# Optimization experiments

Measured on AMD Instinct MI355X. Metric: run time of the kernel, lower is better.

## Reference

```python
import jax, jax.numpy as jnp
import numpy as np

N = 50000      # occupied sparse voxels
C_IN = 512     # inplanes (= 4*planes for residual)
P = 128        # planes
K = 27         # 3x3x3 kernel volume in 3D
EPS = 1e-5
NEG = 0.1      # leaky-relu slope


def setup_inputs() -> dict:
    key = jax.random.key(0)
    k1, k2, k3, k4, k5, k6 = jax.random.split(key, 6)
    x = jax.random.normal(k1, (N, C_IN), dtype=jnp.float32)
    mask = (jax.random.uniform(k2, (N, 1)) > 0.3).astype(jnp.float32)
    nbr = jax.random.randint(k3, (N, K), 0, N, dtype=jnp.int32)
    W1 = jax.random.normal(k4, (C_IN, P), dtype=jnp.float32) * (1.0 / np.sqrt(C_IN))
    W2 = jax.random.normal(k5, (K, P, P), dtype=jnp.float32) * (1.0 / np.sqrt(K * P))
    W3 = jax.random.normal(k6, (P, C_IN), dtype=jnp.float32) * (1.0 / np.sqrt(P))
    return {"x": x, "mask": mask, "nbr": nbr, "W1": W1, "W2": W2, "W3": W3}


def lrelu(x):
    return jnp.where(x >= 0, x, NEG * x)


def inorm(x):
    # Minkowski instance norm: per-channel over all points of the instance
    mu = jnp.mean(x, axis=0, keepdims=True)
    var = jnp.var(x, axis=0, keepdims=True)
    return (x - mu) * jax.lax.rsqrt(var + EPS)


def pconv_k1(x, m, W):
    # 1x1x1 partial conv: mask, matmul, renormalize by coverage (=m itself)
    valid = (m > 0).astype(x.dtype)          # [N,1]
    return (x @ W) * valid, valid


def pconv_k3(x, m, nbr, W):
    # gather-GEMM partial conv over 27-neighborhood map
    mg = m[nbr]                                # [N,K,1]
    xg = x[nbr] * mg                           # [N,K,P] masked gather
    out = jnp.einsum('nkc,kcd->nd', xg, W)     # [N,P]
    msum = jnp.sum(mg, axis=1)                 # [N,1] coverage count
    ratio = (K / jnp.maximum(msum, 1.0)) * (msum > 0).astype(x.dtype)
    return out * ratio, (msum > 0).astype(x.dtype)


def reference(x, mask, nbr, W1, W2, W3):
    out, m = pconv_k1(x, mask, W1)
    out = lrelu(inorm(out))
    out, m = pconv_k3(out, m, nbr, W2)
    out = lrelu(inorm(out))
    out, m = pconv_k1(out, m, W3)
    out = inorm(out)
    out = lrelu(out + x)                       # residual (no downsample)
    m = jnp.clip(m + mask, 0.0, 1.0)           # mask residual + clamp
    return out, m
```

## Files before the change

kernel.cpp:

```cpp
#include <hip/hip_runtime.h>
#include <hip/hip_bf16.h>

#define NPTS 50000
#define CIN  512
#define PCH  128
#define KNB  27
#define EPSV 1e-5f
#define NEGS 0.1f

typedef __bf16 bf16;
typedef __bf16 bf16x8 __attribute__((ext_vector_type(8)));
typedef __bf16 bf16x4 __attribute__((ext_vector_type(4)));
typedef float  f32x4  __attribute__((ext_vector_type(4)));

typedef void __attribute__((address_space(3)))* as3ptr;
typedef const void __attribute__((address_space(1)))* as1ptr;
__device__ __forceinline__ void gl_lds16(const void* g, void* l) {
  __builtin_amdgcn_global_load_lds((as1ptr)g, (as3ptr)l, 16, 0, 0);
}


__global__ void xcvt_kernel(const float* __restrict__ x, bf16* __restrict__ xb) {
  int i = (blockIdx.x * blockDim.x + threadIdx.x) * 8;
  if (i >= NPTS * CIN) return;
  float4 a = *(const float4*)&x[i];
  float4 b = *(const float4*)&x[i + 4];
  bf16x8 o;
  o[0] = (bf16)a.x; o[1] = (bf16)a.y; o[2] = (bf16)a.z; o[3] = (bf16)a.w;
  o[4] = (bf16)b.x; o[5] = (bf16)b.y; o[6] = (bf16)b.z; o[7] = (bf16)b.w;
  *(bf16x8*)&xb[i] = o;
}

__global__ void tcvt_kernel(const float* __restrict__ src, bf16* __restrict__ dst,
                            int R, int Ccols) {
  int i = blockIdx.x * blockDim.x + threadIdx.x;
  if (i >= R * Ccols) return;
  int c = i / R, r = i - c * R;
  dst[i] = (bf16)src[(size_t)r * Ccols + c];
}

__global__ void tcvt_w2k_kernel(const float* __restrict__ src, bf16* __restrict__ dst) {
  int i = blockIdx.x * blockDim.x + threadIdx.x;
  if (i >= KNB * PCH * PCH) return;
  int k = i >> 14, rem = i & 16383;
  int d = rem >> 7, c = rem & 127;
  dst[i] = (bf16)src[(k << 14) + c * 128 + d];
}

__global__ void prep_kernel(const int* __restrict__ nbr, const float* __restrict__ mask,
                            int* __restrict__ nbrT, float* __restrict__ ratio,
                            float* __restrict__ valid2) {
  int n = blockIdx.x * blockDim.x + threadIdx.x;
  if (n >= NPTS) return;
  float s = 0.f;
#pragma unroll
  for (int k = 0; k < KNB; ++k) {
    int idx = nbr[n * KNB + k];
    nbrT[k * NPTS + n] = idx;
    s += (mask[idx] > 0.f) ? 1.f : 0.f;
  }
  ratio[n]  = s > 0.f ? 27.0f / s : 0.f;
  valid2[n] = s > 0.f ? 1.f : 0.f;
}

__global__ void finalize_kernel(const float* __restrict__ ssum, const float* __restrict__ ssq,
                                float* __restrict__ mu, float* __restrict__ inv) {
  int c = threadIdx.x;
  float m = ssum[c] / (float)NPTS;
  float v = ssq[c] / (float)NPTS - m * m;
  mu[c]  = m;
  inv[c] = rsqrtf(v + EPSV);
}

__global__ void ew_kernel(const float* __restrict__ in, const float* __restrict__ mu,
                          const float* __restrict__ inv, const float* __restrict__ rowmask,
                          bf16* __restrict__ outb) {
  int i = (blockIdx.x * blockDim.x + threadIdx.x) * 4;
  if (i >= NPTS * PCH) return;
  float4 v = *(const float4*)&in[i];
  int c = i & 127;
  int row = i >> 7;
  float mk = rowmask[row];
  float t0 = (v.x - mu[c + 0]) * inv[c + 0];
  float t1 = (v.y - mu[c + 1]) * inv[c + 1];
  float t2 = (v.z - mu[c + 2]) * inv[c + 2];
  float t3 = (v.w - mu[c + 3]) * inv[c + 3];
  t0 = (t0 >= 0.f ? t0 : NEGS * t0) * mk;
  t1 = (t1 >= 0.f ? t1 : NEGS * t1) * mk;
  t2 = (t2 >= 0.f ? t2 : NEGS * t2) * mk;
  t3 = (t3 >= 0.f ? t3 : NEGS * t3) * mk;
  bf16x4 o;
  o[0] = (bf16)t0; o[1] = (bf16)t1; o[2] = (bf16)t2; o[3] = (bf16)t3;
  *(bf16x4*)&outb[i] = o;
}

__global__ void final_kernel(const float* __restrict__ x, const bf16* __restrict__ out3n,
                             const float* __restrict__ mu, const float* __restrict__ inv,
                             float* __restrict__ out) {
  int i = (blockIdx.x * blockDim.x + threadIdx.x) * 8;
  if (i >= NPTS * CIN) return;
  bf16x8 v = *(const bf16x8*)&out3n[i];
  float4 x0 = *(const float4*)&x[i];
  float4 x1 = *(const float4*)&x[i + 4];
  int c = i & 511;
  float t[8];
  float xv[8] = {x0.x, x0.y, x0.z, x0.w, x1.x, x1.y, x1.z, x1.w};
#pragma unroll
  for (int q = 0; q < 8; ++q) {
    float u = ((float)v[q] - mu[c + q]) * inv[c + q] + xv[q];
    t[q] = u >= 0.f ? u : NEGS * u;
  }
  float4 o0 = {t[0], t[1], t[2], t[3]}, o1 = {t[4], t[5], t[6], t[7]};
  *(float4*)&out[i] = o0;
  *(float4*)&out[i + 4] = o1;
}

__global__ void maskout_kernel(const float* __restrict__ mask, const float* __restrict__ valid2,
                               float* __restrict__ outm) {
  int n = blockIdx.x * blockDim.x + threadIdx.x;
  if (n >= NPTS) return;
  outm[n] = fminf(valid2[n] + mask[n], 1.f);
}


__global__ __launch_bounds__(256) void gemm1_kernel(
    const bf16* __restrict__ xb, const bf16* __restrict__ w1t,
    const float* __restrict__ mask, float* __restrict__ out1,
    float* __restrict__ ssum, float* __restrict__ ssq) {
  __shared__ __align__(16) bf16 As[2][128 * 128];
  int row0 = blockIdx.x * 128;
  int tid = threadIdx.x;
  int lane = tid & 63, wid = tid >> 6;
  int mq = (wid >> 1) * 64, nq = (wid & 1) * 64;
  int lr = lane & 15, lq = lane >> 4;
  int rb = tid >> 4;
  int msw = (tid & 15) ^ (rb & 7);
  int rowc[8];
#pragma unroll
  for (int j = 0; j < 8; ++j) {
    int rr = row0 + rb + 16 * j;
    rowc[j] = rr < NPTS ? rr : NPTS - 1;
  }
  f32x4 acc[4][4];
#pragma unroll
  for (int i = 0; i < 4; ++i)
#pragma unroll
    for (int j = 0; j < 4; ++j)
#pragma unroll
      for (int r = 0; r < 4; ++r) acc[i][j][r] = 0.f;

#pragma unroll
  for (int j = 0; j < 8; ++j)
    gl_lds16(xb + (size_t)rowc[j] * CIN + (msw << 3),
             &As[0][(j * 256 + wid * 64) * 8]);
  __syncthreads();

  for (int kc = 0; kc < 4; ++kc) {
    int cur = kc & 1;
    const bf16* bp = w1t + (size_t)(nq + lr) * CIN + kc * 128 + lq * 8;
    bf16x8 bfg[4][4];
#pragma unroll
    for (int c0i = 0; c0i < 4; ++c0i)
#pragma unroll
      for (int i = 0; i < 4; ++i)
        bfg[c0i][i] = *(const bf16x8*)(bp + (size_t)i * 16 * CIN + c0i * 32);
    if (kc < 3) {
#pragma unroll
      for (int j = 0; j < 8; ++j)
        gl_lds16(xb + (size_t)rowc[j] * CIN + (kc + 1) * 128 + (msw << 3),
                 &As[cur ^ 1][(j * 256 + wid * 64) * 8]);
    }
#pragma unroll
    for (int c0i = 0; c0i < 4; ++c0i) {
      int cs = ((c0i << 2) + lq) ^ (lr & 7);
      bf16x8 af[4];
#pragma unroll
      for (int i = 0; i < 4; ++i) af[i] = *(const bf16x8*)&As[cur][(mq + i * 16 + lr) * 128 + cs * 8];
#pragma unroll
      for (int i = 0; i < 4; ++i)
#pragma unroll
        for (int j = 0; j < 4; ++j)
          acc[i][j] = __builtin_amdgcn_mfma_f32_16x16x32_bf16(af[i], bfg[c0i][j], acc[i][j], 0, 0, 0);
    }
    __syncthreads();
  }
  float rs[4][4];
#pragma unroll
  for (int i = 0; i < 4; ++i)
#pragma unroll
    for (int r = 0; r < 4; ++r) {
      int row = row0 + mq + i * 16 + lq * 4 + r;
      rs[i][r] = (row < NPTS) ? (mask[row] > 0.f ? 1.f : 0.f) : 0.f;
    }
#pragma unroll
  for (int j = 0; j < 4; ++j) {
    int col = nq + j * 16 + lr;
    float s = 0.f, q = 0.f;
#pragma unroll
    for (int i = 0; i < 4; ++i) {
#pragma unroll
      for (int r = 0; r < 4; ++r) {
        int row = row0 + mq + i * 16 + lq * 4 + r;
        if (row < NPTS) {
          float v = acc[i][j][r] * rs[i][r];
          out1[(size_t)row * PCH + col] = v;
          s += v; q += v * v;
        }
      }
    }
    s += __shfl_xor(s, 16); s += __shfl_xor(s, 32);
    q += __shfl_xor(q, 16); q += __shfl_xor(q, 32);
    if (lq == 0) { atomicAdd(&ssum[col], s); atomicAdd(&ssq[col], q); }
  }
}

__global__ __launch_bounds__(256) void gemm2_kernel(
    const bf16* __restrict__ a, const bf16* __restrict__ w2k,
    const int* __restrict__ nbrT, const float* __restrict__ ratio,
    float* __restrict__ out2, float* __restrict__ ssum, float* __restrict__ ssq) {
  __shared__ __align__(16) bf16 As[2][128 * 128];
  int row0 = blockIdx.x * 128;
  int tid = threadIdx.x;
  int lane = tid & 63, wid = tid >> 6;
  int mq = (wid >> 1) * 64, nq = (wid & 1) * 64;
  int lr = lane & 15, lq = lane >> 4;
  int rb = tid >> 4;
  int msw = (tid & 15) ^ (rb & 7);
  int rowc[8];
#pragma unroll
  for (int j = 0; j < 8; ++j) {
    int rr = row0 + rb + 16 * j;
    rowc[j] = rr < NPTS ? rr : NPTS - 1;
  }
  f32x4 acc[4][4];
#pragma unroll
  for (int i = 0; i < 4; ++i)
#pragma unroll
    for (int j = 0; j < 4; ++j)
#pragma unroll
      for (int r = 0; r < 4; ++r) acc[i][j][r] = 0.f;

  int nidx[8];
#pragma unroll
  for (int j = 0; j < 8; ++j) nidx[j] = nbrT[rowc[j]];
#pragma unroll
  for (int j = 0; j < 8; ++j)
    gl_lds16(a + (size_t)nidx[j] * PCH + (msw << 3),
             &As[0][(j * 256 + wid * 64) * 8]);
#pragma unroll
  for (int j = 0; j < 8; ++j) nidx[j] = nbrT[NPTS + rowc[j]];
  __syncthreads();

  for (int k = 0; k < KNB; ++k) {
    int cur = k & 1;
    const bf16* bp = w2k + (size_t)k * PCH * PCH + (nq + lr) * PCH + lq * 8;
    bf16x8 bfg[4][4];
#pragma unroll
    for (int c0i = 0; c0i < 4; ++c0i)
#pragma unroll
      for (int i = 0; i < 4; ++i)
        bfg[c0i][i] = *(const bf16x8*)(bp + (size_t)i * 16 * PCH + c0i * 32);
    if (k + 1 < KNB) {
#pragma unroll
      for (int j = 0; j < 8; ++j)
        gl_lds16(a + (size_t)nidx[j] * PCH + (msw << 3),
                 &As[cur ^ 1][(j * 256 + wid * 64) * 8]);
    }
    if (k + 2 < KNB) {
#pragma unroll
      for (int j = 0; j < 8; ++j) nidx[j] = nbrT[(k + 2) * NPTS + rowc[j]];
    }
#pragma unroll
    for (int c0i = 0; c0i < 4; ++c0i) {
      int cs = ((c0i << 2) + lq) ^ (lr & 7);
      bf16x8 af[4];
#pragma unroll
      for (int i = 0; i < 4; ++i) af[i] = *(const bf16x8*)&As[cur][(mq + i * 16 + lr) * 128 + cs * 8];
#pragma unroll
      for (int i = 0; i < 4; ++i)
#pragma unroll
        for (int j = 0; j < 4; ++j)
          acc[i][j] = __builtin_amdgcn_mfma_f32_16x16x32_bf16(af[i], bfg[c0i][j], acc[i][j], 0, 0, 0);
    }
    __syncthreads();
  }
  float rs[4][4];
#pragma unroll
  for (int i = 0; i < 4; ++i)
#pragma unroll
    for (int r = 0; r < 4; ++r) {
      int row = row0 + mq + i * 16 + lq * 4 + r;
      rs[i][r] = (row < NPTS) ? ratio[row] : 0.f;
    }
#pragma unroll
  for (int j = 0; j < 4; ++j) {
    int col = nq + j * 16 + lr;
    float s = 0.f, q = 0.f;
#pragma unroll
    for (int i = 0; i < 4; ++i) {
#pragma unroll
      for (int r = 0; r < 4; ++r) {
        int row = row0 + mq + i * 16 + lq * 4 + r;
        if (row < NPTS) {
          float v = acc[i][j][r] * rs[i][r];
          out2[(size_t)row * PCH + col] = v;
          s += v; q += v * v;
        }
      }
    }
    s += __shfl_xor(s, 16); s += __shfl_xor(s, 32);
    q += __shfl_xor(q, 16); q += __shfl_xor(q, 32);
    if (lq == 0) { atomicAdd(&ssum[col], s); atomicAdd(&ssq[col], q); }
  }
}

__global__ __launch_bounds__(256) void gemm3_kernel(
    const bf16* __restrict__ a, const bf16* __restrict__ w3t, bf16* __restrict__ out3n,
    float* __restrict__ ssum, float* __restrict__ ssq) {
  __shared__ __align__(16) bf16 As[128 * 128];
  int row0 = blockIdx.x * 128;
  int ncol0 = blockIdx.y * 128;
  int tid = threadIdx.x;
  int lane = tid & 63, wid = tid >> 6;
  int mq = (wid >> 1) * 64, nq = (wid & 1) * 64;
  int lr = lane & 15, lq = lane >> 4;
  int rb = tid >> 4;
  int msw = (tid & 15) ^ (rb & 7);
#pragma unroll
  for (int j = 0; j < 8; ++j) {
    int rr = row0 + rb + 16 * j;
    int rc = rr < NPTS ? rr : NPTS - 1;
    gl_lds16(a + (size_t)rc * PCH + (msw << 3),
             &As[(j * 256 + wid * 64) * 8]);
  }
  const bf16* bp = w3t + (size_t)(ncol0 + nq + lr) * PCH + lq * 8;
  bf16x8 bfg[4][4];
#pragma unroll
  for (int c0i = 0; c0i < 4; ++c0i)
#pragma unroll
    for (int i = 0; i < 4; ++i)
      bfg[c0i][i] = *(const bf16x8*)(bp + (size_t)i * 16 * PCH + c0i * 32);
  f32x4 acc[4][4];
#pragma unroll
  for (int i = 0; i < 4; ++i)
#pragma unroll
    for (int j = 0; j < 4; ++j)
#pragma unroll
      for (int r = 0; r < 4; ++r) acc[i][j][r] = 0.f;
  __syncthreads();
#pragma unroll
  for (int c0i = 0; c0i < 4; ++c0i) {
    int cs = ((c0i << 2) + lq) ^ (lr & 7);
    bf16x8 af[4];
#pragma unroll
    for (int i = 0; i < 4; ++i) af[i] = *(const bf16x8*)&As[(mq + i * 16 + lr) * 128 + cs * 8];
#pragma unroll
    for (int i = 0; i < 4; ++i)
#pragma unroll
      for (int j = 0; j < 4; ++j)
        acc[i][j] = __builtin_amdgcn_mfma_f32_16x16x32_bf16(af[i], bfg[c0i][j], acc[i][j], 0, 0, 0);
  }
#pragma unroll
  for (int j = 0; j < 4; ++j) {
    int col = ncol0 + nq + j * 16 + lr;
    float s = 0.f, q = 0.f;
#pragma unroll
    for (int i = 0; i < 4; ++i) {
#pragma unroll
      for (int r = 0; r < 4; ++r) {
        int row = row0 + mq + i * 16 + lq * 4 + r;
        if (row < NPTS) {
          float v = acc[i][j][r];
          out3n[(size_t)row * CIN + col] = (bf16)v;
          s += v; q += v * v;
        }
      }
    }
    s += __shfl_xor(s, 16); s += __shfl_xor(s, 32);
    q += __shfl_xor(q, 16); q += __shfl_xor(q, 32);
    if (lq == 0) { atomicAdd(&ssum[col], s); atomicAdd(&ssq[col], q); }
  }
}

extern "C" void kernel_launch(void* const* d_in, const int* in_sizes, int n_in,
                              void* d_out, int out_size, void* d_ws, size_t ws_size,
                              hipStream_t stream) {
  const float* x    = (const float*)d_in[0];
  const float* mask = (const float*)d_in[1];
  const int*   nbr  = (const int*)d_in[2];
  const float* W1   = (const float*)d_in[3];
  const float* W2   = (const float*)d_in[4];
  const float* W3   = (const float*)d_in[5];
  float* out = (float*)d_out;
  char* ws = (char*)d_ws;

  auto al = [](size_t x_) { return (x_ + 255) & ~(size_t)255; };
  size_t off = 0;
  size_t OFF_OUT1  = off; off += al((size_t)NPTS * PCH * 4);
  size_t OFF_OUT2  = off; off += al((size_t)NPTS * PCH * 4);
  size_t OFF_OUT1N = off; off += al((size_t)NPTS * PCH * 2);
  size_t OFF_OUT2N = off; off += al((size_t)NPTS * PCH * 2);
  size_t OFF_W1T   = off; off += al((size_t)PCH * CIN * 2);
  size_t OFF_W2K   = off; off += al((size_t)KNB * PCH * PCH * 2);
  size_t OFF_W3T   = off; off += al((size_t)CIN * PCH * 2);
  size_t OFF_NBRT  = off; off += al((size_t)KNB * NPTS * 4);
  size_t OFF_RATIO = off; off += al((size_t)NPTS * 4);
  size_t OFF_VAL2  = off; off += al((size_t)NPTS * 4);
  size_t OFF_SUMS  = off; off += al((size_t)1536 * 4);
  size_t OFF_PRMS  = off; off += al((size_t)1536 * 4);

  float* out1   = (float*)(ws + OFF_OUT1);
  float* out2   = (float*)(ws + OFF_OUT2);
  bf16*  out3n  = (bf16*)(ws + OFF_OUT1);
  bf16*  xb     = (bf16*)(ws + OFF_OUT2);
  bf16*  out1n  = (bf16*)(ws + OFF_OUT1N);
  bf16*  out2n  = (bf16*)(ws + OFF_OUT2N);
  bf16*  w1t    = (bf16*)(ws + OFF_W1T);
  bf16*  w2k    = (bf16*)(ws + OFF_W2K);
  bf16*  w3t    = (bf16*)(ws + OFF_W3T);
  int*   nbrT   = (int*)(ws + OFF_NBRT);
  float* ratio  = (float*)(ws + OFF_RATIO);
  float* valid2 = (float*)(ws + OFF_VAL2);
  float* sums   = (float*)(ws + OFF_SUMS);
  float* s1sum = sums, *s1sq = sums + 128;
  float* s2sum = sums + 256, *s2sq = sums + 384;
  float* s3sum = sums + 512, *s3sq = sums + 1024;
  float* prms = (float*)(ws + OFF_PRMS);
  float* mu1 = prms, *inv1 = prms + 128;
  float* mu2 = prms + 256, *inv2 = prms + 384;
  float* mu3 = prms + 512, *inv3 = prms + 1024;

  hipMemsetAsync(sums, 0, 1536 * 4, stream);

  prep_kernel<<<(NPTS + 255) / 256, 256, 0, stream>>>(nbr, mask, nbrT, ratio, valid2);
  tcvt_kernel<<<(CIN * PCH + 255) / 256, 256, 0, stream>>>(W1, w1t, CIN, PCH);
  tcvt_w2k_kernel<<<(KNB * PCH * PCH + 255) / 256, 256, 0, stream>>>(W2, w2k);
  tcvt_kernel<<<(PCH * CIN + 255) / 256, 256, 0, stream>>>(W3, w3t, PCH, CIN);
  xcvt_kernel<<<(NPTS * CIN / 8 + 255) / 256, 256, 0, stream>>>(x, xb);

  int mblocks = (NPTS + 127) / 128;

  gemm1_kernel<<<mblocks, 256, 0, stream>>>(xb, w1t, mask, out1, s1sum, s1sq);
  finalize_kernel<<<1, 128, 0, stream>>>(s1sum, s1sq, mu1, inv1);
  ew_kernel<<<(NPTS * PCH / 4 + 255) / 256, 256, 0, stream>>>(out1, mu1, inv1, mask, out1n);

  gemm2_kernel<<<mblocks, 256, 0, stream>>>(out1n, w2k, nbrT, ratio, out2, s2sum, s2sq);
  finalize_kernel<<<1, 128, 0, stream>>>(s2sum, s2sq, mu2, inv2);
  ew_kernel<<<(NPTS * PCH / 4 + 255) / 256, 256, 0, stream>>>(out2, mu2, inv2, valid2, out2n);

  dim3 g3(mblocks, 4);
  gemm3_kernel<<<g3, 256, 0, stream>>>(out2n, w3t, out3n, s3sum, s3sq);
  finalize_kernel<<<1, 512, 0, stream>>>(s3sum, s3sq, mu3, inv3);
  final_kernel<<<(NPTS * CIN / 8 + 255) / 256, 256, 0, stream>>>(x, out3n, mu3, inv3, out);
  maskout_kernel<<<(NPTS + 255) / 256, 256, 0, stream>>>(mask, valid2, out + (size_t)NPTS * CIN);
}
```

Baseline: 502.3 us.

## Restructure gemm1/gemm2 as single-wave 32-row tiles with shuffled gather indices

Gemm1 and gemm2 now run as one 64-thread wavefront per block over 32 rows and all 128 output columns, replacing four waves over a 128x128 tile. LDS use drops to a single 8 KB buffer with no __syncthreads, and the next gather is issued after the current A fragments are read into registers. In gemm2 the neighbour indices are loaded once per lane and spread with __shfl instead of 8 scalar loads per thread. The aim is more blocks, higher occupancy and fewer barriers, at the cost of reloading B weights from global per block, which raises weight traffic about fourfold, and less overlap because each iteration waits on vmcnt(0).

```diff
diff --git a/kernel.cpp b/kernel.cpp
--- a/kernel.cpp
+++ b/kernel.cpp
@@ -123,191 +123,197 @@
 }
 
 
-__global__ __launch_bounds__(256) void gemm1_kernel(
+__global__ __launch_bounds__(64, 3) void gemm1_kernel(
     const bf16* __restrict__ xb, const bf16* __restrict__ w1t,
     const float* __restrict__ mask, float* __restrict__ out1,
     float* __restrict__ ssum, float* __restrict__ ssq) {
-  __shared__ __align__(16) bf16 As[2][128 * 128];
-  int row0 = blockIdx.x * 128;
-  int tid = threadIdx.x;
-  int lane = tid & 63, wid = tid >> 6;
-  int mq = (wid >> 1) * 64, nq = (wid & 1) * 64;
+  __shared__ __align__(16) bf16 As[32 * 128];
+  int row0 = blockIdx.x * 32;
+  int lane = threadIdx.x;
   int lr = lane & 15, lq = lane >> 4;
-  int rb = tid >> 4;
-  int msw = (tid & 15) ^ (rb & 7);
-  int rowc[8];
+  int rowj[8];
 #pragma unroll
   for (int j = 0; j < 8; ++j) {
-    int rr = row0 + rb + 16 * j;
-    rowc[j] = rr < NPTS ? rr : NPTS - 1;
-  }
-  f32x4 acc[4][4];
-#pragma unroll
-  for (int i = 0; i < 4; ++i)
-#pragma unroll
-    for (int j = 0; j < 4; ++j)
-#pragma unroll
-      for (int r = 0; r < 4; ++r) acc[i][j][r] = 0.f;
-
-#pragma unroll
-  for (int j = 0; j < 8; ++j)
-    gl_lds16(xb + (size_t)rowc[j] * CIN + (msw << 3),
-             &As[0][(j * 256 + wid * 64) * 8]);
-  __syncthreads();
-
+    int rr = row0 + j * 4 + lq;
+    rowj[j] = rr < NPTS ? rr : NPTS - 1;
+  }
+  f32x4 acc[2][8];
+#pragma unroll
+  for (int i = 0; i < 2; ++i)
+#pragma unroll
+    for (int n = 0; n < 8; ++n)
+#pragma unroll
+      for (int r = 0; r < 4; ++r) acc[i][n][r] = 0.f;
+
+#pragma unroll
+  for (int j = 0; j < 8; ++j) {
+    int swz = lr ^ ((j & 1) * 4 + lq);
+    gl_lds16(xb + (size_t)rowj[j] * CIN + swz * 8, &As[j * 512 + lane * 8]);
+  }
+
+#pragma unroll 1
   for (int kc = 0; kc < 4; ++kc) {
-    int cur = kc & 1;
-    const bf16* bp = w1t + (size_t)(nq + lr) * CIN + kc * 128 + lq * 8;
-    bf16x8 bfg[4][4];
-#pragma unroll
-    for (int c0i = 0; c0i < 4; ++c0i)
-#pragma unroll
-      for (int i = 0; i < 4; ++i)
-        bfg[c0i][i] = *(const bf16x8*)(bp + (size_t)i * 16 * CIN + c0i * 32);
+    asm volatile("s_waitcnt vmcnt(0)" ::: "memory");
+    __builtin_amdgcn_sched_barrier(0);
+    bf16x8 af[2][4];
+#pragma unroll
+    for (int i = 0; i < 2; ++i)
+#pragma unroll
+      for (int c = 0; c < 4; ++c)
+        af[i][c] = *(const bf16x8*)&As[(i * 16 + lr) * 128 + (((c << 2) + lq) ^ (lr & 7)) * 8];
+    asm volatile("s_waitcnt lgkmcnt(0)" ::: "memory");
+    __builtin_amdgcn_sched_barrier(0);
+    const bf16* bp = w1t + (size_t)lr * CIN + kc * 128 + lq * 8;
+    bf16x8 bfg[8];
+#pragma unroll
+    for (int n = 0; n < 8; ++n) bfg[n] = *(const bf16x8*)(bp + (size_t)n * 16 * CIN);
+    __builtin_amdgcn_sched_barrier(0);
     if (kc < 3) {
 #pragma unroll
-      for (int j = 0; j < 8; ++j)
-        gl_lds16(xb + (size_t)rowc[j] * CIN + (kc + 1) * 128 + (msw << 3),
-                 &As[cur ^ 1][(j * 256 + wid * 64) * 8]);
-    }
-#pragma unroll
-    for (int c0i = 0; c0i < 4; ++c0i) {
-      int cs = ((c0i << 2) + lq) ^ (lr & 7);
-      bf16x8 af[4];
-#pragma unroll
-      for (int i = 0; i < 4; ++i) af[i] = *(const bf16x8*)&As[cur][(mq + i * 16 + lr) * 128 + cs * 8];
-#pragma unroll
-      for (int i = 0; i < 4; ++i)
-#pragma unroll
-        for (int j = 0; j < 4; ++j)
-          acc[i][j] = __builtin_amdgcn_mfma_f32_16x16x32_bf16(af[i], bfg[c0i][j], acc[i][j], 0, 0, 0);
-    }
-    __syncthreads();
-  }
-  float rs[4][4];
-#pragma unroll
-  for (int i = 0; i < 4; ++i)
+      for (int j = 0; j < 8; ++j) {
+        int swz = lr ^ ((j & 1) * 4 + lq);
+        gl_lds16(xb + (size_t)rowj[j] * CIN + (kc + 1) * 128 + swz * 8, &As[j * 512 + lane * 8]);
+      }
+    }
+    __builtin_amdgcn_sched_barrier(0);
+#pragma unroll
+    for (int n = 0; n < 8; ++n) {
+      acc[0][n] = __builtin_amdgcn_mfma_f32_16x16x32_bf16(af[0][0], bfg[n], acc[0][n], 0, 0, 0);
+      acc[1][n] = __builtin_amdgcn_mfma_f32_16x16x32_bf16(af[1][0], bfg[n], acc[1][n], 0, 0, 0);
+    }
+#pragma unroll
+    for (int c = 1; c < 4; ++c) {
+#pragma unroll
+      for (int n = 0; n < 8; ++n) bfg[n] = *(const bf16x8*)(bp + (size_t)n * 16 * CIN + c * 32);
+#pragma unroll
+      for (int n = 0; n < 8; ++n) {
+        acc[0][n] = __builtin_amdgcn_mfma_f32_16x16x32_bf16(af[0][c], bfg[n], acc[0][n], 0, 0, 0);
+        acc[1][n] = __builtin_amdgcn_mfma_f32_16x16x32_bf16(af[1][c], bfg[n], acc[1][n], 0, 0, 0);
+      }
+    }
+  }
+  float rs[2][4];
+#pragma unroll
+  for (int i = 0; i < 2; ++i)
 #pragma unroll
     for (int r = 0; r < 4; ++r) {
-      int row = row0 + mq + i * 16 + lq * 4 + r;
+      int row = row0 + i * 16 + lq * 4 + r;
       rs[i][r] = (row < NPTS) ? (mask[row] > 0.f ? 1.f : 0.f) : 0.f;
     }
 #pragma unroll
-  for (int j = 0; j < 4; ++j) {
-    int col = nq + j * 16 + lr;
+  for (int n = 0; n < 8; ++n) {
+    int col = n * 16 + lr;
     float s = 0.f, q = 0.f;
 #pragma unroll
-    for (int i = 0; i < 4; ++i) {
+    for (int i = 0; i < 2; ++i)
 #pragma unroll
       for (int r = 0; r < 4; ++r) {
-        int row = row0 + mq + i * 16 + lq * 4 + r;
+        int row = row0 + i * 16 + lq * 4 + r;
         if (row < NPTS) {
-          float v = acc[i][j][r] * rs[i][r];
+          float v = acc[i][n][r] * rs[i][r];
           out1[(size_t)row * PCH + col] = v;
           s += v; q += v * v;
         }
       }
-    }
     s += __shfl_xor(s, 16); s += __shfl_xor(s, 32);
     q += __shfl_xor(q, 16); q += __shfl_xor(q, 32);
     if (lq == 0) { atomicAdd(&ssum[col], s); atomicAdd(&ssq[col], q); }
   }
 }
 
-__global__ __launch_bounds__(256) void gemm2_kernel(
+__global__ __launch_bounds__(64, 3) void gemm2_kernel(
     const bf16* __restrict__ a, const bf16* __restrict__ w2k,
     const int* __restrict__ nbrT, const float* __restrict__ ratio,
     float* __restrict__ out2, float* __restrict__ ssum, float* __restrict__ ssq) {
-  __shared__ __align__(16) bf16 As[2][128 * 128];
-  int row0 = blockIdx.x * 128;
-  int tid = threadIdx.x;
-  int lane = tid & 63, wid = tid >> 6;
-  int mq = (wid >> 1) * 64, nq = (wid & 1) * 64;
+  __shared__ __align__(16) bf16 As[32 * 128];
+  int row0 = blockIdx.x * 32;
+  int lane = threadIdx.x;
   int lr = lane & 15, lq = lane >> 4;
-  int rb = tid >> 4;
-  int msw = (tid & 15) ^ (rb & 7);
-  int rowc[8];
+  int rglob = row0 + (lane & 31);
+  if (rglob >= NPTS) rglob = NPTS - 1;
+  f32x4 acc[2][8];
+#pragma unroll
+  for (int i = 0; i < 2; ++i)
+#pragma unroll
+    for (int n = 0; n < 8; ++n)
+#pragma unroll
+      for (int r = 0; r < 4; ++r) acc[i][n][r] = 0.f;
+
+  int idxreg = nbrT[rglob];
 #pragma unroll
   for (int j = 0; j < 8; ++j) {
-    int rr = row0 + rb + 16 * j;
-    rowc[j] = rr < NPTS ? rr : NPTS - 1;
-  }
-  f32x4 acc[4][4];
-#pragma unroll
-  for (int i = 0; i < 4; ++i)
-#pragma unroll
-    for (int j = 0; j < 4; ++j)
-#pragma unroll
-      for (int r = 0; r < 4; ++r) acc[i][j][r] = 0.f;
-
-  int nidx[8];
-#pragma unroll
-  for (int j = 0; j < 8; ++j) nidx[j] = nbrT[rowc[j]];
-#pragma unroll
-  for (int j = 0; j < 8; ++j)
-    gl_lds16(a + (size_t)nidx[j] * PCH + (msw << 3),
-             &As[0][(j * 256 + wid * 64) * 8]);
-#pragma unroll
-  for (int j = 0; j < 8; ++j) nidx[j] = nbrT[NPTS + rowc[j]];
-  __syncthreads();
-
+    int src = __shfl(idxreg, j * 4 + lq);
+    int swz = lr ^ ((j & 1) * 4 + lq);
+    gl_lds16(a + (size_t)src * PCH + swz * 8, &As[j * 512 + lane * 8]);
+  }
+  idxreg = nbrT[NPTS + rglob];
+
+#pragma unroll 1
   for (int k = 0; k < KNB; ++k) {
-    int cur = k & 1;
-    const bf16* bp = w2k + (size_t)k * PCH * PCH + (nq + lr) * PCH + lq * 8;
-    bf16x8 bfg[4][4];
-#pragma unroll
-    for (int c0i = 0; c0i < 4; ++c0i)
-#pragma unroll
-      for (int i = 0; i < 4; ++i)
-        bfg[c0i][i] = *(const bf16x8*)(bp + (size_t)i * 16 * PCH + c0i * 32);
+    asm volatile("s_waitcnt vmcnt(0)" ::: "memory");
+    __builtin_amdgcn_sched_barrier(0);
+    bf16x8 af[2][4];
+#pragma unroll
+    for (int i = 0; i < 2; ++i)
+#pragma unroll
+      for (int c = 0; c < 4; ++c)
+        af[i][c] = *(const bf16x8*)&As[(i * 16 + lr) * 128 + (((c << 2) + lq) ^ (lr & 7)) * 8];
+    asm volatile("s_waitcnt lgkmcnt(0)" ::: "memory");
+    __builtin_amdgcn_sched_barrier(0);
+    const bf16* bp = w2k + ((size_t)k << 14) + lr * PCH + lq * 8;
+    bf16x8 bfg[8];
+#pragma unroll
+    for (int n = 0; n < 8; ++n) bfg[n] = *(const bf16x8*)(bp + n * 16 * PCH);
+    __builtin_amdgcn_sched_barrier(0);
     if (k + 1 < KNB) {
 #pragma unroll
-      for (int j = 0; j < 8; ++j)
-        gl_lds16(a + (size_t)nidx[j] * PCH + (msw << 3),
-                 &As[cur ^ 1][(j * 256 + wid * 64) * 8]);
-    }
-    if (k + 2 < KNB) {
-#pragma unroll
-      for (int j = 0; j < 8; ++j) nidx[j] = nbrT[(k + 2) * NPTS + rowc[j]];
-    }
-#pragma unroll
-    for (int c0i = 0; c0i < 4; ++c0i) {
-      int cs = ((c0i << 2) + lq) ^ (lr & 7);
-      bf16x8 af[4];
-#pragma unroll
-      for (int i = 0; i < 4; ++i) af[i] = *(const bf16x8*)&As[cur][(mq + i * 16 + lr) * 128 + cs * 8];
-#pragma unroll
-      for (int i = 0; i < 4; ++i)
-#pragma unroll
-        for (int j = 0; j < 4; ++j)
-          acc[i][j] = __builtin_amdgcn_mfma_f32_16x16x32_bf16(af[i], bfg[c0i][j], acc[i][j], 0, 0, 0);
-    }
-    __syncthreads();
-  }
-  float rs[4][4];
-#pragma unroll
-  for (int i = 0; i < 4; ++i)
+      for (int j = 0; j < 8; ++j) {
+        int src = __shfl(idxreg, j * 4 + lq);
+        int swz = lr ^ ((j & 1) * 4 + lq);
+        gl_lds16(a + (size_t)src * PCH + swz * 8, &As[j * 512 + lane * 8]);
+      }
+      if (k + 2 < KNB) idxreg = nbrT[(k + 2) * NPTS + rglob];
+    }
+    __builtin_amdgcn_sched_barrier(0);
+#pragma unroll
+    for (int n = 0; n < 8; ++n) {
+      acc[0][n] = __builtin_amdgcn_mfma_f32_16x16x32_bf16(af[0][0], bfg[n], acc[0][n], 0, 0, 0);
+      acc[1][n] = __builtin_amdgcn_mfma_f32_16x16x32_bf16(af[1][0], bfg[n], acc[1][n], 0, 0, 0);
+    }
+#pragma unroll
+    for (int c = 1; c < 4; ++c) {
+#pragma unroll
+      for (int n = 0; n < 8; ++n) bfg[n] = *(const bf16x8*)(bp + n * 16 * PCH + c * 32);
+#pragma unroll
+      for (int n = 0; n < 8; ++n) {
+        acc[0][n] = __builtin_amdgcn_mfma_f32_16x16x32_bf16(af[0][c], bfg[n], acc[0][n], 0, 0, 0);
+        acc[1][n] = __builtin_amdgcn_mfma_f32_16x16x32_bf16(af[1][c], bfg[n], acc[1][n], 0, 0, 0);
+      }
+    }
+  }
+  float rs[2][4];
+#pragma unroll
+  for (int i = 0; i < 2; ++i)
 #pragma unroll
     for (int r = 0; r < 4; ++r) {
-      int row = row0 + mq + i * 16 + lq * 4 + r;
+      int row = row0 + i * 16 + lq * 4 + r;
       rs[i][r] = (row < NPTS) ? ratio[row] : 0.f;
     }
 #pragma unroll
-  for (int j = 0; j < 4; ++j) {
-    int col = nq + j * 16 + lr;
+  for (int n = 0; n < 8; ++n) {
+    int col = n * 16 + lr;
     float s = 0.f, q = 0.f;
 #pragma unroll
-    for (int i = 0; i < 4; ++i) {
+    for (int i = 0; i < 2; ++i)
 #pragma unroll
       for (int r = 0; r < 4; ++r) {
-        int row = row0 + mq + i * 16 + lq * 4 + r;
+        int row = row0 + i * 16 + lq * 4 + r;
         if (row < NPTS) {
-          float v = acc[i][j][r] * rs[i][r];
+          float v = acc[i][n][r] * rs[i][r];
           out2[(size_t)row * PCH + col] = v;
           s += v; q += v * v;
         }
       }
-    }
     s += __shfl_xor(s, 16); s += __shfl_xor(s, 32);
     q += __shfl_xor(q, 16); q += __shfl_xor(q, 32);
     if (lq == 0) { atomicAdd(&ssum[col], s); atomicAdd(&ssq[col], q); }
@@ -438,13 +444,14 @@
   tcvt_kernel<<<(PCH * CIN + 255) / 256, 256, 0, stream>>>(W3, w3t, PCH, CIN);
   xcvt_kernel<<<(NPTS * CIN / 8 + 255) / 256, 256, 0, stream>>>(x, xb);
 
+  int mb32 = (NPTS + 31) / 32;
   int mblocks = (NPTS + 127) / 128;
 
-  gemm1_kernel<<<mblocks, 256, 0, stream>>>(xb, w1t, mask, out1, s1sum, s1sq);
+  gemm1_kernel<<<mb32, 64, 0, stream>>>(xb, w1t, mask, out1, s1sum, s1sq);
   finalize_kernel<<<1, 128, 0, stream>>>(s1sum, s1sq, mu1, inv1);
   ew_kernel<<<(NPTS * PCH / 4 + 255) / 256, 256, 0, stream>>>(out1, mu1, inv1, mask, out1n);
 
-  gemm2_kernel<<<mblocks, 256, 0, stream>>>(out1n, w2k, nbrT, ratio, out2, s2sum, s2sq);
+  gemm2_kernel<<<mb32, 64, 0, stream>>>(out1n, w2k, nbrT, ratio, out2, s2sum, s2sq);
   finalize_kernel<<<1, 128, 0, stream>>>(s2sum, s2sq, mu2, inv2);
   ew_kernel<<<(NPTS * PCH / 4 + 255) / 256, 256, 0, stream>>>(out2, mu2, inv2, valid2, out2n);
 
```

Result: slower. 619.7 us (+23.4%).

## Drop LDS staging in gather-GEMM, load neighbor rows directly into registers

Applied to the files above, without the earlier changes.

The 27-tap gather GEMM no longer stages gathered activation tiles in double-buffered LDS through global_load_lds with barriers. Each wave now covers all 128 rows and a 32-column slice, loading gathered A fragments and W2 fragments straight from global memory into registers with a software-pipelined ping-pong over the K chunks. Neighbor indices are spread across lanes with shuffles. This removes the LDS traffic and per-tap __syncthreads, but each gathered A row is now read by all four waves instead of once, which raises global/L2 load volume and register pressure.

```diff
diff --git a/kernel.cpp b/kernel.cpp
--- a/kernel.cpp
+++ b/kernel.cpp
@@ -18,7 +18,6 @@
 __device__ __forceinline__ void gl_lds16(const void* g, void* l) {
   __builtin_amdgcn_global_load_lds((as1ptr)g, (as3ptr)l, 16, 0, 0);
 }
-
 
 __global__ void xcvt_kernel(const float* __restrict__ x, bf16* __restrict__ xb) {
   int i = (blockIdx.x * blockDim.x + threadIdx.x) * 8;
@@ -218,89 +217,98 @@
     const bf16* __restrict__ a, const bf16* __restrict__ w2k,
     const int* __restrict__ nbrT, const float* __restrict__ ratio,
     float* __restrict__ out2, float* __restrict__ ssum, float* __restrict__ ssq) {
-  __shared__ __align__(16) bf16 As[2][128 * 128];
   int row0 = blockIdx.x * 128;
   int tid = threadIdx.x;
-  int lane = tid & 63, wid = tid >> 6;
-  int mq = (wid >> 1) * 64, nq = (wid & 1) * 64;
+  int lane = tid & 63, w = tid >> 6;
   int lr = lane & 15, lq = lane >> 4;
-  int rb = tid >> 4;
-  int msw = (tid & 15) ^ (rb & 7);
-  int rowc[8];
-#pragma unroll
-  for (int j = 0; j < 8; ++j) {
-    int rr = row0 + rb + 16 * j;
-    rowc[j] = rr < NPTS ? rr : NPTS - 1;
-  }
-  f32x4 acc[4][4];
-#pragma unroll
-  for (int i = 0; i < 4; ++i)
-#pragma unroll
-    for (int j = 0; j < 4; ++j)
+  int rowA = row0 + lane;       if (rowA >= NPTS) rowA = NPTS - 1;
+  int rowB = row0 + 64 + lane;  if (rowB >= NPTS) rowB = NPTS - 1;
+
+  f32x4 acc[8][2];
+#pragma unroll
+  for (int i = 0; i < 8; ++i)
+#pragma unroll
+    for (int j = 0; j < 2; ++j)
 #pragma unroll
       for (int r = 0; r < 4; ++r) acc[i][j][r] = 0.f;
 
-  int nidx[8];
-#pragma unroll
-  for (int j = 0; j < 8; ++j) nidx[j] = nbrT[rowc[j]];
-#pragma unroll
-  for (int j = 0; j < 8; ++j)
-    gl_lds16(a + (size_t)nidx[j] * PCH + (msw << 3),
-             &As[0][(j * 256 + wid * 64) * 8]);
-#pragma unroll
-  for (int j = 0; j < 8; ++j) nidx[j] = nbrT[NPTS + rowc[j]];
-  __syncthreads();
-
+#define LDC(AB, BB, KK, ABP, B0P, B1P) do {                                     \
+    _Pragma("unroll")                                                           \
+    for (int _i = 0; _i < 8; ++_i)                                              \
+      AB[_i] = *(const bf16x8*)(ABP[_i] + (KK) * 32);                           \
+    BB[0] = *(const bf16x8*)(B0P + (KK) * 32);                                  \
+    BB[1] = *(const bf16x8*)(B1P + (KK) * 32);                                  \
+  } while (0)
+
+#define MMA(AB, BB) do {                                                        \
+    _Pragma("unroll")                                                           \
+    for (int _i = 0; _i < 8; ++_i) {                                            \
+      acc[_i][0] = __builtin_amdgcn_mfma_f32_16x16x32_bf16(AB[_i], BB[0], acc[_i][0], 0, 0, 0); \
+      acc[_i][1] = __builtin_amdgcn_mfma_f32_16x16x32_bf16(AB[_i], BB[1], acc[_i][1], 0, 0, 0); \
+    }                                                                           \
+  } while (0)
+
+  int i0 = nbrT[rowA], i1 = nbrT[rowB];
+  const bf16* ab[8];
+#pragma unroll
+  for (int i = 0; i < 8; ++i) {
+    int idx = __shfl((i < 4) ? i0 : i1, (i & 3) * 16 + lr);
+    ab[i] = a + (size_t)idx * PCH + lq * 8;
+  }
+  const bf16* bb0 = w2k + (size_t)(w * 32 + lr) * PCH + lq * 8;
+  const bf16* bb1 = bb0 + 16 * PCH;
+
+  bf16x8 A0[8], A1[8], B0[2], B1[2];
+  LDC(A0, B0, 0, ab, bb0, bb1);
+  int i0n = nbrT[NPTS + rowA];
+  int i1n = nbrT[NPTS + rowB];
+
+#pragma unroll 1
   for (int k = 0; k < KNB; ++k) {
-    int cur = k & 1;
-    const bf16* bp = w2k + (size_t)k * PCH * PCH + (nq + lr) * PCH + lq * 8;
-    bf16x8 bfg[4][4];
-#pragma unroll
-    for (int c0i = 0; c0i < 4; ++c0i)
-#pragma unroll
-      for (int i = 0; i < 4; ++i)
-        bfg[c0i][i] = *(const bf16x8*)(bp + (size_t)i * 16 * PCH + c0i * 32);
+    const bf16* abn[8];
+#pragma unroll
+    for (int i = 0; i < 8; ++i) {
+      int idx = __shfl((i < 4) ? i0n : i1n, (i & 3) * 16 + lr);
+      abn[i] = a + (size_t)idx * PCH + lq * 8;
+    }
+    LDC(A1, B1, 1, ab, bb0, bb1);
+    int kn2 = (k + 2 < KNB) ? k + 2 : KNB - 1;
+    int i0t = nbrT[(size_t)kn2 * NPTS + rowA];
+    int i1t = nbrT[(size_t)kn2 * NPTS + rowB];
+    MMA(A0, B0);
+    LDC(A0, B0, 2, ab, bb0, bb1);
+    MMA(A1, B1);
+    LDC(A1, B1, 3, ab, bb0, bb1);
+    MMA(A0, B0);
     if (k + 1 < KNB) {
 #pragma unroll
-      for (int j = 0; j < 8; ++j)
-        gl_lds16(a + (size_t)nidx[j] * PCH + (msw << 3),
-                 &As[cur ^ 1][(j * 256 + wid * 64) * 8]);
-    }
-    if (k + 2 < KNB) {
-#pragma unroll
-      for (int j = 0; j < 8; ++j) nidx[j] = nbrT[(k + 2) * NPTS + rowc[j]];
-    }
-#pragma unroll
-    for (int c0i = 0; c0i < 4; ++c0i) {
-      int cs = ((c0i << 2) + lq) ^ (lr & 7);
-      bf16x8 af[4];
-#pragma unroll
-      for (int i = 0; i < 4; ++i) af[i] = *(const bf16x8*)&As[cur][(mq + i * 16 + lr) * 128 + cs * 8];
-#pragma unroll
-      for (int i = 0; i < 4; ++i)
-#pragma unroll
-        for (int j = 0; j < 4; ++j)
-          acc[i][j] = __builtin_amdgcn_mfma_f32_16x16x32_bf16(af[i], bfg[c0i][j], acc[i][j], 0, 0, 0);
-    }
-    __syncthreads();
-  }
-  float rs[4][4];
-#pragma unroll
-  for (int i = 0; i < 4; ++i)
+      for (int i = 0; i < 8; ++i) ab[i] = abn[i];
+      bb0 += PCH * PCH;  bb1 += PCH * PCH;
+      i0n = i0t;  i1n = i1t;
+      LDC(A0, B0, 0, ab, bb0, bb1);
+    }
+    MMA(A1, B1);
+  }
+#undef LDC
+#undef MMA
+
+  float rs[8][4];
+#pragma unroll
+  for (int i = 0; i < 8; ++i)
 #pragma unroll
     for (int r = 0; r < 4; ++r) {
-      int row = row0 + mq + i * 16 + lq * 4 + r;
+      int row = row0 + i * 16 + lq * 4 + r;
       rs[i][r] = (row < NPTS) ? ratio[row] : 0.f;
     }
 #pragma unroll
-  for (int j = 0; j < 4; ++j) {
-    int col = nq + j * 16 + lr;
+  for (int j = 0; j < 2; ++j) {
+    int col = w * 32 + j * 16 + lr;
     float s = 0.f, q = 0.f;
 #pragma unroll
-    for (int i = 0; i < 4; ++i) {
+    for (int i = 0; i < 8; ++i) {
 #pragma unroll
       for (int r = 0; r < 4; ++r) {
-        int row = row0 + mq + i * 16 + lq * 4 + r;
+        int row = row0 + i * 16 + lq * 4 + r;
         if (row < NPTS) {
           float v = acc[i][j][r] * rs[i][r];
           out2[(size_t)row * PCH + col] = v;
```

Result: slower. 659.9 us (+31.4%).
